# Kernel optimization log

Hardware: AMD Instinct MI355X
Metric: run time of the kernel (lower is better)

The kernel has to match this reference:

```python
import jax, jax.numpy as jnp
import numpy as np

N, E = 50000, 800000
D_IN, D_H, D_OUT = 128, 128, 64


def _gcn_conv(h, src, dst, norm, b, n):
    # h already linearly transformed: aggregate norm-weighted messages to dst
    msg = h[src] * norm[:, None]                      # [E+N, d]
    out = jax.ops.segment_sum(msg, dst, num_segments=n)
    return out + b


def setup_inputs() -> dict:
    key = jax.random.key(0)
    ks = jax.random.split(key, 5)
    x = jax.random.normal(ks[0], (N, D_IN), jnp.float32)
    edge_index = jax.random.randint(ks[1], (2, E), 0, N, jnp.int32)
    s1 = 1.0 / np.sqrt(D_IN)
    s2 = 1.0 / np.sqrt(D_H)
    W1 = jax.random.uniform(ks[2], (D_IN, D_H), jnp.float32, -s1, s1)
    b1 = jnp.zeros((D_H,), jnp.float32)
    W2 = jax.random.uniform(ks[3], (D_H, D_OUT), jnp.float32, -s2, s2)
    b2 = jnp.zeros((D_OUT,), jnp.float32)
    return {"x": x, "edge_index": edge_index, "W1": W1, "b1": b1, "W2": W2, "b2": b2}


def reference(x, edge_index, W1, b1, W2, b2):
    n = x.shape[0]
    loops = jnp.arange(n, dtype=edge_index.dtype)
    src = jnp.concatenate([edge_index[0], loops])     # add self-loops
    dst = jnp.concatenate([edge_index[1], loops])
    # symmetric normalization D^{-1/2} (A+I) D^{-1/2}; deg is in-degree incl. self-loop
    deg = jax.ops.segment_sum(jnp.ones(dst.shape[0], x.dtype), dst, num_segments=n)
    dinv = jnp.where(deg > 0, jax.lax.rsqrt(deg), 0.0)
    norm = dinv[src] * dinv[dst]
    h = _gcn_conv(x @ W1, src, dst, norm, b1, n)
    h = jax.nn.relu(h)                                # dropout = identity (eval)
    out = _gcn_conv(h @ W2, src, dst, norm, b2, n)
    return out
```

## Files before the change

kernel.cpp:

```cpp
#include <hip/hip_runtime.h>

typedef __bf16 bf16x8 __attribute__((ext_vector_type(8)));
typedef float  f32x4  __attribute__((ext_vector_type(4)));
typedef unsigned long long u64;

constexpr int PAD       = 64;
constexpr int BIN_SHIFT = 9;
constexpr int CAP       = 12288;
constexpr int SUBS      = 4;
constexpr int NPS       = 128;
constexpr int STR       = 68;


template<bool IN_BF16, int NC>
__global__ __launch_bounds__(256) void fused_bin_gemm_k(
    const int* __restrict__ src, const int* __restrict__ dst,
    int* __restrict__ bincur, u64* __restrict__ bin_data, int E, int fillB,
    const void* __restrict__ Xv, const float* __restrict__ W,
    __bf16* __restrict__ C, int n) {
  constexpr int K   = 128;
  constexpr int KP  = K + 8;
  constexpr int NT  = NC / 16;
  constexpr int KC  = K / 32;

  __shared__ __bf16 WT[NC * KP];
  __shared__ int hist[128];
  __shared__ int hbase[128];

  if ((int)blockIdx.x < fillB) {
    const int NB = (n + ((1 << BIN_SHIFT) - 1)) >> BIN_SHIFT;
    if (threadIdx.x < 128) hist[threadIdx.x] = 0;
    __syncthreads();

    int base_e = (blockIdx.x * 256 + threadIdx.x) * 4;
    int m = E - base_e;
    m = m < 0 ? 0 : (m > 4 ? 4 : m);

    int sa[4], da[4], ba[4], pa[4];
    if (m == 4) {
      int4 s4 = *reinterpret_cast<const int4*>(src + base_e);
      int4 d4 = *reinterpret_cast<const int4*>(dst + base_e);
      sa[0] = s4.x; sa[1] = s4.y; sa[2] = s4.z; sa[3] = s4.w;
      da[0] = d4.x; da[1] = d4.y; da[2] = d4.z; da[3] = d4.w;
    } else {
      for (int k = 0; k < m; ++k) { sa[k] = src[base_e + k]; da[k] = dst[base_e + k]; }
    }
    for (int k = 0; k < m; ++k) {
      ba[k] = da[k] >> BIN_SHIFT;
      pa[k] = atomicAdd(&hist[ba[k]], 1);
    }
    __syncthreads();
    if ((int)threadIdx.x < NB)
      hbase[threadIdx.x] = atomicAdd(&bincur[threadIdx.x], hist[threadIdx.x]);
    __syncthreads();
    for (int k = 0; k < m; ++k) {
      int pos = hbase[ba[k]] + pa[k];
      if (pos < CAP)
        bin_data[(size_t)ba[k] * CAP + pos] = ((u64)(unsigned)sa[k] << 32) | (unsigned)da[k];
    }
    return;
  }

  for (int idx = threadIdx.x; idx < K * (NC / 4); idx += 256) {
    int k  = idx / (NC / 4);
    int c4 = idx % (NC / 4);
    f32x4 v = reinterpret_cast<const f32x4*>(W)[idx];
    WT[(c4 * 4 + 0) * KP + k] = (__bf16)v[0];
    WT[(c4 * 4 + 1) * KP + k] = (__bf16)v[1];
    WT[(c4 * 4 + 2) * KP + k] = (__bf16)v[2];
    WT[(c4 * 4 + 3) * KP + k] = (__bf16)v[3];
  }
  __syncthreads();

  const int lane = threadIdx.x & 63;
  const int lr = lane & 15;
  const int lg = lane >> 4;

  bf16x8 bfrag[NT][KC];
#pragma unroll
  for (int nt = 0; nt < NT; ++nt)
#pragma unroll
    for (int kc = 0; kc < KC; ++kc)
      bfrag[nt][kc] = *reinterpret_cast<const bf16x8*>(
          &WT[(nt * 16 + lr) * KP + kc * 32 + lg * 8]);

  const int vb = blockIdx.x - fillB;
  const int gw = vb * 4 + (threadIdx.x >> 6);
  const int nw = (gridDim.x - fillB) * 4;
  const int mtiles = (n + 15) / 16;

  for (int mt = gw; mt < mtiles; mt += nw) {
    const int row  = mt * 16 + lr;
    const int crow = (row < n) ? row : (n - 1);

    bf16x8 afrag[KC];
#pragma unroll
    for (int kc = 0; kc < KC; ++kc) {
      if constexpr (IN_BF16) {
        afrag[kc] = *reinterpret_cast<const bf16x8*>(
            (const __bf16*)Xv + (size_t)crow * K + kc * 32 + lg * 8);
      } else {
        const f32x4* p = reinterpret_cast<const f32x4*>(
            (const float*)Xv + (size_t)crow * K + kc * 32 + lg * 8);
        f32x4 v0 = p[0], v1 = p[1];
        bf16x8 a;
        a[0] = (__bf16)v0[0]; a[1] = (__bf16)v0[1];
        a[2] = (__bf16)v0[2]; a[3] = (__bf16)v0[3];
        a[4] = (__bf16)v1[0]; a[5] = (__bf16)v1[1];
        a[6] = (__bf16)v1[2]; a[7] = (__bf16)v1[3];
        afrag[kc] = a;
      }
    }

    f32x4 acc[NT];
#pragma unroll
    for (int nt = 0; nt < NT; ++nt) acc[nt] = (f32x4){0.f, 0.f, 0.f, 0.f};
#pragma unroll
    for (int kc = 0; kc < KC; ++kc)
#pragma unroll
      for (int nt = 0; nt < NT; ++nt)
        acc[nt] = __builtin_amdgcn_mfma_f32_16x16x32_bf16(afrag[kc], bfrag[nt][kc],
                                                          acc[nt], 0, 0, 0);

#pragma unroll
    for (int nt = 0; nt < NT; ++nt)
#pragma unroll
      for (int r = 0; r < 4; ++r) {
        int orow = mt * 16 + lg * 4 + r;
        if (orow < n) C[(size_t)orow * NC + nt * 16 + lr] = (__bf16)acc[nt][r];
      }
  }
}


__global__ __launch_bounds__(512) void csr_build_k(const int* __restrict__ bincur,
                                                   const u64* __restrict__ bin_data,
                                                   int* __restrict__ srcs_pad,
                                                   int* __restrict__ cnt,
                                                   float* __restrict__ dinv,
                                                   __bf16* __restrict__ h1b, int n) {
  __shared__ int rows[NPS * STR];
  __shared__ int lcnt[NPS];

  const int bin = blockIdx.x / SUBS;
  const int sub = blockIdx.x % SUBS;
  const int lo  = (bin << BIN_SHIFT) + sub * NPS;
  const int hi  = min(n, (bin + 1) << BIN_SHIFT);

  for (int i = threadIdx.x; i < NPS * STR; i += 512) rows[i] = 0;
  for (int i = threadIdx.x; i < NPS; i += 512) lcnt[i] = 0;
  __syncthreads();

  int cntE = bincur[bin];
  cntE = cntE < CAP ? cntE : CAP;
  const u64* bd = bin_data + (size_t)bin * CAP;

  for (int i = threadIdx.x; i < cntE; i += 512) {
    u64 p = bd[i];
    int d = (int)(p & 0xffffffffu);
    unsigned l = (unsigned)(d - lo);
    if (l < (unsigned)NPS) {
      int q = atomicAdd(&lcnt[l], 1);
      if (q < PAD) rows[l * STR + q] = (int)(p >> 32);
    }
  }
  __syncthreads();

  for (int i = threadIdx.x; i < NPS * (PAD / 4); i += 512) {
    int nl = i >> 4;
    int c4 = i & 15;
    int g = lo + nl;
    if (g < hi)
      *reinterpret_cast<int4*>(&srcs_pad[(size_t)g * PAD + c4 * 4]) =
          *reinterpret_cast<const int4*>(&rows[nl * STR + c4 * 4]);
  }
  for (int i = threadIdx.x; i < NPS; i += 512) {
    int g = lo + i;
    if (g < hi) {
      int c = lcnt[i];
      cnt[g] = c;
      dinv[g] = rsqrtf((float)(c + 1));
    }
  }
  bf16x8* h8 = reinterpret_cast<bf16x8*>(h1b);
  for (int i = threadIdx.x; i < NPS * 16; i += 512) {
    int nl = i >> 4;
    int c8 = i & 15;
    int g = lo + nl;
    if (g < hi) {
      float di = rsqrtf((float)(lcnt[nl] + 1));
      bf16x8 v = h8[(size_t)g * 16 + c8];
      bf16x8 o;
#pragma unroll
      for (int q = 0; q < 8; ++q) o[q] = (__bf16)((float)v[q] * di);
      h8[(size_t)g * 16 + c8] = o;
    }
  }
}


template<bool IN_BF16, int NC, bool SCALE>
__global__ __launch_bounds__(256) void gemm_mfma_k(const void* __restrict__ Xv,
                                                   const float* __restrict__ W,
                                                   __bf16* __restrict__ C, int n,
                                                   const float* __restrict__ rowscale) {
  constexpr int K   = 128;
  constexpr int KP  = K + 8;
  constexpr int NT  = NC / 16;
  constexpr int KC  = K / 32;

  __shared__ __bf16 WT[NC * KP];
  for (int idx = threadIdx.x; idx < K * (NC / 4); idx += 256) {
    int k  = idx / (NC / 4);
    int c4 = idx % (NC / 4);
    f32x4 v = reinterpret_cast<const f32x4*>(W)[idx];
    WT[(c4 * 4 + 0) * KP + k] = (__bf16)v[0];
    WT[(c4 * 4 + 1) * KP + k] = (__bf16)v[1];
    WT[(c4 * 4 + 2) * KP + k] = (__bf16)v[2];
    WT[(c4 * 4 + 3) * KP + k] = (__bf16)v[3];
  }
  __syncthreads();

  const int lane = threadIdx.x & 63;
  const int lr = lane & 15;
  const int lg = lane >> 4;

  bf16x8 bfrag[NT][KC];
#pragma unroll
  for (int nt = 0; nt < NT; ++nt)
#pragma unroll
    for (int kc = 0; kc < KC; ++kc)
      bfrag[nt][kc] = *reinterpret_cast<const bf16x8*>(
          &WT[(nt * 16 + lr) * KP + kc * 32 + lg * 8]);

  const int gw = blockIdx.x * 4 + (threadIdx.x >> 6);
  const int nw = gridDim.x * 4;
  const int mtiles = (n + 15) / 16;

  for (int mt = gw; mt < mtiles; mt += nw) {
    const int row  = mt * 16 + lr;
    const int crow = (row < n) ? row : (n - 1);

    bf16x8 afrag[KC];
#pragma unroll
    for (int kc = 0; kc < KC; ++kc) {
      if constexpr (IN_BF16) {
        afrag[kc] = *reinterpret_cast<const bf16x8*>(
            (const __bf16*)Xv + (size_t)crow * K + kc * 32 + lg * 8);
      } else {
        const f32x4* p = reinterpret_cast<const f32x4*>(
            (const float*)Xv + (size_t)crow * K + kc * 32 + lg * 8);
        f32x4 v0 = p[0], v1 = p[1];
        bf16x8 a;
        a[0] = (__bf16)v0[0]; a[1] = (__bf16)v0[1];
        a[2] = (__bf16)v0[2]; a[3] = (__bf16)v0[3];
        a[4] = (__bf16)v1[0]; a[5] = (__bf16)v1[1];
        a[6] = (__bf16)v1[2]; a[7] = (__bf16)v1[3];
        afrag[kc] = a;
      }
    }

    f32x4 acc[NT];
#pragma unroll
    for (int nt = 0; nt < NT; ++nt) acc[nt] = (f32x4){0.f, 0.f, 0.f, 0.f};
#pragma unroll
    for (int kc = 0; kc < KC; ++kc)
#pragma unroll
      for (int nt = 0; nt < NT; ++nt)
        acc[nt] = __builtin_amdgcn_mfma_f32_16x16x32_bf16(afrag[kc], bfrag[nt][kc],
                                                          acc[nt], 0, 0, 0);

#pragma unroll
    for (int r = 0; r < 4; ++r) {
      int orow = mt * 16 + lg * 4 + r;
      if (orow < n) {
        float sc = SCALE ? rowscale[orow] : 1.0f;
#pragma unroll
        for (int nt = 0; nt < NT; ++nt)
          C[(size_t)orow * NC + nt * 16 + lr] = (__bf16)(acc[nt][r] * sc);
      }
    }
  }
}


template<int D, bool RELU_OUT, bool OUT_BF16>
__global__ __launch_bounds__(256) void gather_bf_k(const __bf16* __restrict__ h,
                                                   const int* __restrict__ cnt,
                                                   const int* __restrict__ srcs_pad,
                                                   const float* __restrict__ dinv,
                                                   const float* __restrict__ bias,
                                                   void* __restrict__ outv, int n) {
  constexpr int L = D / 8;
  int t = blockIdx.x * 256 + threadIdx.x;
  int node = t / L;
  int d8 = t % L;
  if (node >= n) return;

  int c = cnt[node];
  c = c < PAD ? c : PAD;
  const int* row = srcs_pad + (size_t)node * PAD;
  const bf16x8* h8 = reinterpret_cast<const bf16x8*>(h);

  float acc[8];
#pragma unroll
  for (int q = 0; q < 8; ++q) acc[q] = 0.f;

  const int cf = c & ~3;
  for (int j0 = 0; j0 < cf; j0 += 4) {
    int4 s4 = *reinterpret_cast<const int4*>(row + j0);
    bf16x8 v0 = h8[(size_t)s4.x * L + d8];
    bf16x8 v1 = h8[(size_t)s4.y * L + d8];
    bf16x8 v2 = h8[(size_t)s4.z * L + d8];
    bf16x8 v3 = h8[(size_t)s4.w * L + d8];
#pragma unroll
    for (int q = 0; q < 8; ++q)
      acc[q] += (float)v0[q] + (float)v1[q] + (float)v2[q] + (float)v3[q];
  }
  for (int j = cf; j < c; ++j) {
    int s = row[j];
    bf16x8 v = h8[(size_t)s * L + d8];
#pragma unroll
    for (int q = 0; q < 8; ++q) acc[q] += (float)v[q];
  }

  const float di = dinv[node];
  bf16x8 sv = h8[(size_t)node * L + d8];

  float o[8];
#pragma unroll
  for (int q = 0; q < 8; ++q) {
    float b = bias[d8 * 8 + q];
    float val = (acc[q] + (float)sv[q]) * di + b;
    o[q] = RELU_OUT ? fmaxf(val, 0.f) : val;
  }

  if (OUT_BF16) {
    bf16x8 ov;
#pragma unroll
    for (int q = 0; q < 8; ++q) ov[q] = (__bf16)o[q];
    reinterpret_cast<bf16x8*>(outv)[(size_t)node * L + d8] = ov;
  } else {
    f32x4 lo = {o[0], o[1], o[2], o[3]};
    f32x4 hi = {o[4], o[5], o[6], o[7]};
    f32x4* op = reinterpret_cast<f32x4*>((float*)outv + (size_t)node * D + d8 * 8);
    op[0] = lo;
    op[1] = hi;
  }
}


extern "C" void kernel_launch(void* const* d_in, const int* in_sizes, int n_in,
                              void* d_out, int out_size, void* d_ws, size_t ws_size,
                              hipStream_t stream) {
  const float* x  = (const float*)d_in[0];
  const int*   ei = (const int*)d_in[1];
  const float* W1 = (const float*)d_in[2];
  const float* b1 = (const float*)d_in[3];
  const float* W2 = (const float*)d_in[4];
  const float* b2 = (const float*)d_in[5];

  const int n = in_sizes[0] / 128;
  const int E = in_sizes[1] / 2;
  const int* src = ei;
  const int* dst = ei + E;
  float* out = (float*)d_out;

  const int NB = (n + ((1 << BIN_SHIFT) - 1)) >> BIN_SHIFT;

  int*   bincur   = (int*)d_ws;
  int*   cnt      = (int*)d_ws + 128;
  float* dinv     = (float*)d_ws + 128 + n;
  int*   srcs_pad = (int*)d_ws + 128 + 2 * n;
  size_t w = (size_t)128 + 2 * n + (size_t)n * PAD;
  __bf16* h1b   = (__bf16*)((int*)d_ws + w);   w += (size_t)n * 64;
  __bf16* agg1b = (__bf16*)((int*)d_ws + w);   w += (size_t)n * 64;
  __bf16* h3b   = (__bf16*)((int*)d_ws + w);
  u64* bin_data = (u64*)agg1b;

  hipMemsetAsync(bincur, 0, 128 * sizeof(int), stream);

  const int fillB = (E / 4 + 255) / 256;
  fused_bin_gemm_k<false, 128><<<fillB + 512, 256, 0, stream>>>(
      src, dst, bincur, bin_data, E, fillB, x, W1, h1b, n);

  csr_build_k<<<NB * SUBS, 512, 0, stream>>>(bincur, bin_data, srcs_pad, cnt, dinv, h1b, n);

  {
    long long t = (long long)n * 16;
    gather_bf_k<128, true, true><<<(int)((t + 255) / 256), 256, 0, stream>>>(
        h1b, cnt, srcs_pad, dinv, b1, agg1b, n);
  }

  gemm_mfma_k<true, 64, true><<<512, 256, 0, stream>>>(agg1b, W2, h3b, n, dinv);
  {
    long long t = (long long)n * 8;
    gather_bf_k<64, false, false><<<(int)((t + 255) / 256), 256, 0, stream>>>(
        h3b, cnt, srcs_pad, dinv, b2, out, n);
  }
}
```

Baseline: 109.8 us.

## Stage binned edges in shared memory and pad gather rows with zero sentinel

The edge-binning blocks now sort their edges by bin in shared memory with a prefix scan before writing to global bins, so each bin's stores become contiguous and coalesced instead of scattered. CSR rows are padded with a sentinel index n pointing to an appended zero row in h1b/h3b, which lets the gather loop process 8 neighbours per iteration with no remainder loop. The sentinel rows are zeroed by a new init kernel that replaces the memset. This adds extra LDS work, barriers and a larger workspace, and wasted loads for padded slots.

```diff
diff --git a/kernel.cpp b/kernel.cpp
--- a/kernel.cpp
+++ b/kernel.cpp
@@ -10,6 +10,15 @@
 constexpr int SUBS      = 4;
 constexpr int NPS       = 128;
 constexpr int STR       = 68;
+
+
+__global__ void init_k(int* __restrict__ bincur, __bf16* __restrict__ h1zero,
+                       __bf16* __restrict__ h3zero) {
+  int t = threadIdx.x;
+  if (t < 128) bincur[t] = 0;
+  h1zero[t] = (__bf16)0.f;
+  if (t < 64) h3zero[t] = (__bf16)0.f;
+}
 
 
 template<bool IN_BF16, int NC>
@@ -23,20 +32,26 @@
   constexpr int NT  = NC / 16;
   constexpr int KC  = K / 32;
 
-  __shared__ __bf16 WT[NC * KP];
-  __shared__ int hist[128];
-  __shared__ int hbase[128];
+  __shared__ __align__(16) char smem[NC * KP * 2];
 
   if ((int)blockIdx.x < fillB) {
+    u64* pairs = (u64*)smem;
+    int* binof = (int*)(smem + 8192);
+    int* hist  = (int*)(smem + 12288);
+    int* cur   = (int*)(smem + 12800);
+    int* sbase = (int*)(smem + 13312);
+    int* gbase = (int*)(smem + 13824);
     const int NB = (n + ((1 << BIN_SHIFT) - 1)) >> BIN_SHIFT;
-    if (threadIdx.x < 128) hist[threadIdx.x] = 0;
+    const int t = threadIdx.x;
+
+    if (t < 128) { hist[t] = 0; cur[t] = 0; }
     __syncthreads();
 
-    int base_e = (blockIdx.x * 256 + threadIdx.x) * 4;
+    int base_e = (blockIdx.x * 256 + t) * 4;
     int m = E - base_e;
     m = m < 0 ? 0 : (m > 4 ? 4 : m);
 
-    int sa[4], da[4], ba[4], pa[4];
+    int sa[4], da[4], ba[4];
     if (m == 4) {
       int4 s4 = *reinterpret_cast<const int4*>(src + base_e);
       int4 d4 = *reinterpret_cast<const int4*>(dst + base_e);
@@ -47,20 +62,42 @@
     }
     for (int k = 0; k < m; ++k) {
       ba[k] = da[k] >> BIN_SHIFT;
-      pa[k] = atomicAdd(&hist[ba[k]], 1);
+      atomicAdd(&hist[ba[k]], 1);
     }
     __syncthreads();
-    if ((int)threadIdx.x < NB)
-      hbase[threadIdx.x] = atomicAdd(&bincur[threadIdx.x], hist[threadIdx.x]);
+
+    if (t < 128) sbase[t] = hist[t];
     __syncthreads();
+    for (int off = 1; off < 128; off <<= 1) {
+      int u = (t >= off && t < 128) ? sbase[t - off] : 0;
+      __syncthreads();
+      if (t < 128) sbase[t] += u;
+      __syncthreads();
+    }
+    if (t < NB) gbase[t] = atomicAdd(&bincur[t], hist[t]);
+    if (t < 128) sbase[t] -= hist[t];
+    __syncthreads();
+
     for (int k = 0; k < m; ++k) {
-      int pos = hbase[ba[k]] + pa[k];
-      if (pos < CAP)
-        bin_data[(size_t)ba[k] * CAP + pos] = ((u64)(unsigned)sa[k] << 32) | (unsigned)da[k];
+      int b = ba[k];
+      int q = atomicAdd(&cur[b], 1);
+      int slot = sbase[b] + q;
+      pairs[slot] = ((u64)(unsigned)sa[k] << 32) | (unsigned)da[k];
+      binof[slot] = b;
+    }
+    __syncthreads();
+
+    int T = E - blockIdx.x * 1024;
+    T = T > 1024 ? 1024 : T;
+    for (int i = t; i < T; i += 256) {
+      int b = binof[i];
+      int pos = gbase[b] + (i - sbase[b]);
+      if (pos < CAP) bin_data[(size_t)b * CAP + pos] = pairs[i];
     }
     return;
   }
 
+  __bf16* WT = (__bf16*)smem;
   for (int idx = threadIdx.x; idx < K * (NC / 4); idx += 256) {
     int k  = idx / (NC / 4);
     int c4 = idx % (NC / 4);
@@ -147,7 +184,7 @@
   const int lo  = (bin << BIN_SHIFT) + sub * NPS;
   const int hi  = min(n, (bin + 1) << BIN_SHIFT);
 
-  for (int i = threadIdx.x; i < NPS * STR; i += 512) rows[i] = 0;
+  for (int i = threadIdx.x; i < NPS * STR; i += 512) rows[i] = n;
   for (int i = threadIdx.x; i < NPS; i += 512) lcnt[i] = 0;
   __syncthreads();
 
@@ -299,33 +336,31 @@
 
   int c = cnt[node];
   c = c < PAD ? c : PAD;
+  const float di = dinv[node];
   const int* row = srcs_pad + (size_t)node * PAD;
   const bf16x8* h8 = reinterpret_cast<const bf16x8*>(h);
+  bf16x8 sv = h8[(size_t)node * L + d8];
 
   float acc[8];
 #pragma unroll
   for (int q = 0; q < 8; ++q) acc[q] = 0.f;
 
-  const int cf = c & ~3;
-  for (int j0 = 0; j0 < cf; j0 += 4) {
-    int4 s4 = *reinterpret_cast<const int4*>(row + j0);
-    bf16x8 v0 = h8[(size_t)s4.x * L + d8];
-    bf16x8 v1 = h8[(size_t)s4.y * L + d8];
-    bf16x8 v2 = h8[(size_t)s4.z * L + d8];
-    bf16x8 v3 = h8[(size_t)s4.w * L + d8];
+  for (int j0 = 0; j0 < c; j0 += 8) {
+    int4 a = *reinterpret_cast<const int4*>(row + j0);
+    int4 b = *reinterpret_cast<const int4*>(row + j0 + 4);
+    bf16x8 v0 = h8[(size_t)a.x * L + d8];
+    bf16x8 v1 = h8[(size_t)a.y * L + d8];
+    bf16x8 v2 = h8[(size_t)a.z * L + d8];
+    bf16x8 v3 = h8[(size_t)a.w * L + d8];
+    bf16x8 v4 = h8[(size_t)b.x * L + d8];
+    bf16x8 v5 = h8[(size_t)b.y * L + d8];
+    bf16x8 v6 = h8[(size_t)b.z * L + d8];
+    bf16x8 v7 = h8[(size_t)b.w * L + d8];
 #pragma unroll
     for (int q = 0; q < 8; ++q)
-      acc[q] += (float)v0[q] + (float)v1[q] + (float)v2[q] + (float)v3[q];
-  }
-  for (int j = cf; j < c; ++j) {
-    int s = row[j];
-    bf16x8 v = h8[(size_t)s * L + d8];
-#pragma unroll
-    for (int q = 0; q < 8; ++q) acc[q] += (float)v[q];
-  }
-
-  const float di = dinv[node];
-  bf16x8 sv = h8[(size_t)node * L + d8];
+      acc[q] += ((float)v0[q] + (float)v1[q]) + ((float)v2[q] + (float)v3[q]) +
+                ((float)v4[q] + (float)v5[q]) + ((float)v6[q] + (float)v7[q]);
+  }
 
   float o[8];
 #pragma unroll
@@ -373,12 +408,12 @@
   float* dinv     = (float*)d_ws + 128 + n;
   int*   srcs_pad = (int*)d_ws + 128 + 2 * n;
   size_t w = (size_t)128 + 2 * n + (size_t)n * PAD;
-  __bf16* h1b   = (__bf16*)((int*)d_ws + w);   w += (size_t)n * 64;
+  __bf16* h1b   = (__bf16*)((int*)d_ws + w);   w += (size_t)(n + 1) * 64;
   __bf16* agg1b = (__bf16*)((int*)d_ws + w);   w += (size_t)n * 64;
   __bf16* h3b   = (__bf16*)((int*)d_ws + w);
   u64* bin_data = (u64*)agg1b;
 
-  hipMemsetAsync(bincur, 0, 128 * sizeof(int), stream);
+  init_k<<<1, 128, 0, stream>>>(bincur, h1b + (size_t)n * 128, h3b + (size_t)n * 64);
 
   const int fillB = (E / 4 + 255) / 256;
   fused_bin_gemm_k<false, 128><<<fillB + 512, 256, 0, stream>>>(
```

Result: no change. 109.9 us (+0.1%).
